# Kernel optimization log

Measured on AMD Instinct MI355X. Metric: run time of the kernel, lower is better.

The kernel has to match this reference:

```python
import jax, jax.numpy as jnp
import numpy as np


def setup_inputs() -> dict:
    key = jax.random.key(0)
    k1, k2, k3 = jax.random.split(key, 3)
    B, N, D, T = 8, 2, 256, 500
    SPK = 2000
    H = jax.random.normal(k1, (B, N, D, T), dtype=jnp.float32)
    S = jax.random.randint(k2, (B, N, T), 0, SPK, dtype=jnp.int64)
    E = jax.random.normal(k3, (SPK, D), dtype=jnp.float32)
    alpha = jnp.ones((1,), dtype=jnp.float32) * 10.0
    beta = jnp.ones((1,), dtype=jnp.float32) * 5.0
    return {"H": H, "S": S, "E": E, "alpha": alpha, "beta": beta, "N": 2}


def reference(H, S, E, alpha, beta, N):
    # H: (B, N, D, T); S: (B, N, T) int ids; E: (SPK, D)
    B, N_, D, T = H.shape
    # embedding lookup: (B, N, T, D) -> (B, N, D, T)
    E_S = jnp.transpose(E[S], (0, 1, 3, 2))
    # pairwise dist between predicted vectors and active-speaker embeddings
    # (B, N_pred=N, N_emb=N, T) -- small, direct broadcast
    Dist_p = jnp.sum((H[:, None, :, :, :] - E_S[:, :, None, :, :]) ** 2, axis=3)
    # N == 2 path matching (identity vs swap), min over the two alignments
    p0 = Dist_p[:, 0, 0, :] + Dist_p[:, 1, 1, :]  # (B, T)
    p1 = Dist_p[:, 0, 1, :] + Dist_p[:, 1, 0, :]  # (B, T)
    Dmin = jnp.minimum(p0, p1)                    # (B, T)
    Dmin = -alpha * Dmin + beta                   # broadcast (1,) over (B, T)
    # full distance to every speaker: ||H||^2 + ||E||^2 - 2 H.E
    # avoids materializing (B, SPK, N, D, T)
    Hsq = jnp.sum(H * H, axis=2)                  # (B, N, T)
    Esq = jnp.sum(E * E, axis=1)                  # (SPK,)
    cross = jnp.einsum('bndt,sd->bsnt', H, E)     # (B, SPK, N, T)
    Dist = Hsq[:, None, :, :] + Esq[None, :, None, None] - 2.0 * cross
    Dist = -alpha * Dist + beta                   # (B, SPK, N, T)
    lse = jax.nn.logsumexp(Dist, axis=1)          # (B, N, T)
    loss = -jnp.mean(Dmin) + jnp.mean(lse)
    return (E_S[:, :, :, 0], loss)
```

## Files before the change

### kernel.cpp

```cpp
#include <hip/hip_runtime.h>
#include <math.h>

#define Bb   8
#define Dd   256
#define Tt   500
#define SPK  2000
#define SPKP 2048
#define BN   16
#define L2E  1.4426950408889634f
#define LN2  0.6931471805599453f

#define EXP2F(x) __builtin_amdgcn_exp2f(x)
#define LOG2F(x) __builtin_amdgcn_logf(x)

#define F_ESN   0
#define F_HSQP  4096
#define F_PM    36864
#define F_PL    69632
#define F_DMP2  102400
#define EBF_BYTES ((size_t)167936 * 4)
#define HBF_BYTES (EBF_BYTES + (size_t)1048576)

#define ROWSTRIDE 264

typedef __bf16 v8bf __attribute__((ext_vector_type(8)));
typedef float  v4f  __attribute__((ext_vector_type(4)));

__device__ inline unsigned pack_bf16x2(float lo, float hi) {
    union { __bf16 h; unsigned short u; } a, b;
    a.h = (__bf16)lo; b.h = (__bf16)hi;
    return ((unsigned)b.u << 16) | (unsigned)a.u;
}

__global__ __launch_bounds__(256) void prep_all_kernel(
        const float* __restrict__ E, const int* __restrict__ S,
        const float* __restrict__ H, const float* __restrict__ alpha,
        const float* __restrict__ beta, float* __restrict__ ws,
        float* __restrict__ out) {
    int bid = blockIdx.x;
    int tid = threadIdx.x;

    if (bid < 512) {
        int s = bid * 4 + (tid >> 6);
        int lane = tid & 63;
        float4 v = make_float4(0.f, 0.f, 0.f, 0.f);
        if (s < SPK) v = ((const float4*)E)[s * 64 + lane];
        __bf16* ebf = (__bf16*)((char*)ws + EBF_BYTES);
        uint2 pp;
        pp.x = pack_bf16x2(v.x, v.y);
        pp.y = pack_bf16x2(v.z, v.w);
        *(uint2*)(ebf + (size_t)s * Dd + lane * 4) = pp;
        float acc = v.x * v.x + v.y * v.y + v.z * v.z + v.w * v.w;
        #pragma unroll
        for (int off = 32; off > 0; off >>= 1) acc += __shfl_down(acc, off, 64);
        if (lane == 0) ws[F_ESN + s] = (s < SPK) ? (-alpha[0] * acc * L2E) : -1e30f;
    } else if (bid < 528) {
        if (bid == 512 && tid == 0) out[BN * Dd] = 0.f;
        int i = (bid - 512) * 256 + tid;
        int bn = i >> 8, d = i & 255;
        out[i] = E[(size_t)S[bn * Tt] * Dd + d];
    } else {
        __shared__ float trans[32][65];
        int u = bid - 528;
        int bn = u >> 6;
        int r = u & 63;
        int tt0 = (r & 15) * 32;
        int d0 = (r >> 4) * 64;
        const float* Hb = H + (size_t)bn * Dd * Tt;
        #pragma unroll
        for (int p = 0; p < 8; ++p) {
            int flat = p * 256 + tid;
            int dd = flat >> 5;
            int tl = flat & 31;
            int t = tt0 + tl;
            trans[tl][dd] = (t < Tt) ? Hb[(size_t)(d0 + dd) * Tt + t] : 0.f;
        }
        __syncthreads();
        int tw = tid >> 3;
        int j = tid & 7;
        int t = tt0 + tw;
        bool ok = (t < Tt);
        int tc = ok ? t : (Tt - 1);
        int b = bn >> 1;
        int s0 = S[(b * 2 + 0) * Tt + tc];
        int s1 = S[(b * 2 + 1) * Tt + tc];
        const float4* e0p = (const float4*)(E + (size_t)s0 * Dd + d0 + j * 8);
        const float4* e1p = (const float4*)(E + (size_t)s1 * Dd + d0 + j * 8);
        float4 ea0 = e0p[0], ea1 = e0p[1];
        float4 eb0 = e1p[0], eb1 = e1p[1];
        float ev0[8] = {ea0.x, ea0.y, ea0.z, ea0.w, ea1.x, ea1.y, ea1.z, ea1.w};
        float ev1[8] = {eb0.x, eb0.y, eb0.z, eb0.w, eb1.x, eb1.y, eb1.z, eb1.w};
        float sq = 0.f, p0 = 0.f, p1 = 0.f;
        float vals[8];
        #pragma unroll
        for (int e = 0; e < 8; ++e) {
            float x = trans[tw][j * 8 + e];
            vals[e] = x;
            sq = fmaf(x, x, sq);
            float u0 = x - ev0[e]; p0 = fmaf(u0, u0, p0);
            float u1 = x - ev1[e]; p1 = fmaf(u1, u1, p1);
        }
        sq += __shfl_xor(sq, 1, 64); p0 += __shfl_xor(p0, 1, 64); p1 += __shfl_xor(p1, 1, 64);
        sq += __shfl_xor(sq, 2, 64); p0 += __shfl_xor(p0, 2, 64); p1 += __shfl_xor(p1, 2, 64);
        sq += __shfl_xor(sq, 4, 64); p0 += __shfl_xor(p0, 4, 64); p1 += __shfl_xor(p1, 4, 64);
        uint4 pk;
        pk.x = pack_bf16x2(vals[0], vals[1]);
        pk.y = pack_bf16x2(vals[2], vals[3]);
        pk.z = pack_bf16x2(vals[4], vals[5]);
        pk.w = pack_bf16x2(vals[6], vals[7]);
        __bf16* hbf = (__bf16*)((char*)ws + HBF_BYTES);
        *(uint4*)(hbf + ((size_t)(bn * 512 + t) * Dd + d0 + j * 8)) = pk;
        if (j == 0) {
            ws[F_HSQP + (size_t)(bn * 512 + t) * 4 + (r >> 4)] = sq;
            if (ok) {
                float2 pr = make_float2(p0, p1);
                *(float2*)(ws + F_DMP2 + (((size_t)bn * 512 + t) * 4 + (r >> 4)) * 2) = pr;
            }
        }
    }
}

__global__ __launch_bounds__(256, 2) void lse_mfma_kernel(
        const float* __restrict__ alpha, const float* __restrict__ beta,
        float* __restrict__ ws) {
    __shared__ __bf16 shB[64 * ROWSTRIDE];
    __shared__ __bf16 shA[4 * 16 * ROWSTRIDE];
    __shared__ float mrg_m[4][4][16], mrg_l[4][4][16];

    int bn = blockIdx.x;
    int t0 = blockIdx.y * 64;
    int mz = blockIdx.z;
    int tid = threadIdx.x;
    int lane = tid & 63;
    int n = lane & 15;
    int q = lane >> 4;
    int w = tid >> 6;

    const __bf16* ebf = (const __bf16*)((const char*)ws + EBF_BYTES);
    const __bf16* hbf = (const __bf16*)((const char*)ws + HBF_BYTES);

    #pragma unroll
    for (int p = 0; p < 8; ++p) {
        int flat = p * 256 + tid;
        int row = flat >> 5;
        int ch = flat & 31;
        uint4 vb = *(const uint4*)(hbf + ((size_t)(bn * 512 + t0 + row) * Dd + ch * 8));
        *(uint4*)(shB + row * ROWSTRIDE + ch * 8) = vb;
    }
    __syncthreads();

    v8bf bq[4][8];
    #pragma unroll
    for (int i = 0; i < 4; ++i) {
        int tloc = 16 * i + n;
        #pragma unroll
        for (int ks = 0; ks < 8; ++ks) {
            bq[i][ks] = *reinterpret_cast<const v8bf*>(&shB[tloc * ROWSTRIDE + ks * 32 + q * 8]);
        }
    }

    float A = alpha[0], Bv = beta[0];
    float ta2p = 2.f * A * L2E;
    float ctc2[4];
    #pragma unroll
    for (int i = 0; i < 4; ++i) {
        int t = t0 + 16 * i + n;
        float4 hq = *(const float4*)(ws + F_HSQP + (size_t)(bn * 512 + t) * 4);
        float hs = hq.x + hq.y + hq.z + hq.w;
        ctc2[i] = (t < Tt) ? ((Bv - A * hs) * L2E) : 0.f;
    }

    float lm[4], ll[4];
    #pragma unroll
    for (int i = 0; i < 4; ++i) { lm[i] = -INFINITY; ll[i] = 0.f; }

    __bf16* shAw = shA + w * (16 * ROWSTRIDE);

    for (int c = 0; c < 8; ++c) {
        int sbase = mz * 512 + c * 64 + w * 16;

        uint4 tmp[8];
        #pragma unroll
        for (int p = 0; p < 8; ++p) {
            int flat = p * 64 + lane;
            int row = flat >> 5;
            int ch = flat & 31;
            tmp[p] = *(const uint4*)(ebf + ((size_t)(sbase + row) * Dd + ch * 8));
        }
        #pragma unroll
        for (int p = 0; p < 8; ++p) {
            int flat = p * 64 + lane;
            int row = flat >> 5;
            int ch = flat & 31;
            *(uint4*)(shAw + row * ROWSTRIDE + ch * 8) = tmp[p];
        }
        __asm__ volatile("s_waitcnt lgkmcnt(0)" ::: "memory");

        v8bf af[8];
        #pragma unroll
        for (int ks = 0; ks < 8; ++ks) {
            af[ks] = *reinterpret_cast<const v8bf*>(&shAw[n * ROWSTRIDE + ks * 32 + q * 8]);
        }
        float4 es4 = *(const float4*)(ws + F_ESN + sbase - w * 16 + w * 16 + q * 4);

        v4f acc[4];
        #pragma unroll
        for (int i = 0; i < 4; ++i) acc[i] = (v4f){0.f, 0.f, 0.f, 0.f};
        #pragma unroll
        for (int ks = 0; ks < 8; ++ks) {
            #pragma unroll
            for (int i = 0; i < 4; ++i) {
                acc[i] = __builtin_amdgcn_mfma_f32_16x16x32_bf16(af[ks], bq[i][ks], acc[i], 0, 0, 0);
            }
        }
        float e0 = es4.x, e1 = es4.y, e2 = es4.z, e3 = es4.w;
        #pragma unroll
        for (int i = 0; i < 4; ++i) {
            float c2 = ctc2[i];
            float v0 = fmaf(ta2p, acc[i][0], c2 + e0);
            float v1 = fmaf(ta2p, acc[i][1], c2 + e1);
            float v2 = fmaf(ta2p, acc[i][2], c2 + e2);
            float v3 = fmaf(ta2p, acc[i][3], c2 + e3);
            float vm = fmaxf(fmaxf(v0, v1), fmaxf(v2, v3));
            float s = EXP2F(v0 - vm) + EXP2F(v1 - vm) + EXP2F(v2 - vm) + EXP2F(v3 - vm);
            float nm = fmaxf(lm[i], vm);
            ll[i] = ll[i] * EXP2F(lm[i] - nm) + s * EXP2F(vm - nm);
            lm[i] = nm;
        }
    }

    #pragma unroll
    for (int i = 0; i < 4; ++i) {
        float m = lm[i], l = ll[i];
        #pragma unroll
        for (int msk = 16; msk <= 32; msk <<= 1) {
            float om = __shfl_xor(m, msk, 64);
            float ol = __shfl_xor(l, msk, 64);
            float nm = fmaxf(m, om);
            l = l * EXP2F(m - nm) + ol * EXP2F(om - nm);
            m = nm;
        }
        if (q == 0) { mrg_m[w][i][n] = m; mrg_l[w][i][n] = l; }
    }
    __syncthreads();

    if (tid < 64) {
        int i = tid >> 4, cc = tid & 15;
        float m = mrg_m[0][i][cc], l = mrg_l[0][i][cc];
        #pragma unroll
        for (int wv = 1; wv < 4; ++wv) {
            float om = mrg_m[wv][i][cc], ol = mrg_l[wv][i][cc];
            float nm = fmaxf(m, om);
            l = l * EXP2F(m - nm) + ol * EXP2F(om - nm);
            m = nm;
        }
        int tw = t0 + 16 * i + cc;
        if (tw < Tt) {
            ws[F_PM + (bn * 512 + tw) * 4 + mz] = m;
            ws[F_PL + (bn * 512 + tw) * 4 + mz] = l;
        }
    }
}

__global__ __launch_bounds__(512) void final_kernel(
        const float* __restrict__ alpha, const float* __restrict__ beta,
        const float* __restrict__ ws, float* __restrict__ out) {
    __shared__ float rL[8], rD[8];
    int b = blockIdx.x;
    int tid = threadIdx.x;
    float A = alpha[0], Bv = beta[0];

    float lsum = 0.f, dsum = 0.f;
    int t = tid;
    if (t < Tt) {
        #pragma unroll
        for (int nn = 0; nn < 2; ++nn) {
            int idx = (b * 2 + nn) * 512 + t;
            float4 m4 = *(const float4*)(ws + F_PM + (size_t)idx * 4);
            float4 l4 = *(const float4*)(ws + F_PL + (size_t)idx * 4);
            float m = m4.x, l = l4.x, nm;
            nm = fmaxf(m, m4.y); l = l * EXP2F(m - nm) + l4.y * EXP2F(m4.y - nm); m = nm;
            nm = fmaxf(m, m4.z); l = l * EXP2F(m - nm) + l4.z * EXP2F(m4.z - nm); m = nm;
            nm = fmaxf(m, m4.w); l = l * EXP2F(m - nm) + l4.w * EXP2F(m4.w - nm); m = nm;
            lsum += LN2 * (m + LOG2F(l));
        }
        const float4* P0 = (const float4*)(ws + F_DMP2 + ((size_t)(2 * b + 0) * 512 + t) * 8);
        const float4* P1 = (const float4*)(ws + F_DMP2 + ((size_t)(2 * b + 1) * 512 + t) * 8);
        float4 a0 = P0[0], a1 = P0[1];
        float4 b0 = P1[0], b1 = P1[1];
        float d00 = a0.x + a0.z + a1.x + a1.z;
        float d01 = a0.y + a0.w + a1.y + a1.w;
        float d10 = b0.x + b0.z + b1.x + b1.z;
        float d11 = b0.y + b0.w + b1.y + b1.w;
        float dm = fminf(d00 + d11, d01 + d10);
        dsum = -A * dm + Bv;
    }

    int lane = tid & 63, w = tid >> 6;
    #pragma unroll
    for (int off = 32; off > 0; off >>= 1) {
        lsum += __shfl_down(lsum, off, 64);
        dsum += __shfl_down(dsum, off, 64);
    }
    if (lane == 0) { rL[w] = lsum; rD[w] = dsum; }
    __syncthreads();
    if (tid == 0) {
        float L = 0.f, D = 0.f;
        #pragma unroll
        for (int wv = 0; wv < 8; ++wv) { L += rL[wv]; D += rD[wv]; }
        atomicAdd(&out[BN * Dd], -(D / (float)(Bb * Tt)) + L / (float)(BN * Tt));
    }
}

extern "C" void kernel_launch(void* const* d_in, const int* in_sizes, int n_in,
                              void* d_out, int out_size, void* d_ws, size_t ws_size,
                              hipStream_t stream) {
    const float* H     = (const float*)d_in[0];
    const int*   S     = (const int*)d_in[1];
    const float* E     = (const float*)d_in[2];
    const float* alpha = (const float*)d_in[3];
    const float* beta  = (const float*)d_in[4];
    float* out = (float*)d_out;
    float* ws  = (float*)d_ws;

    prep_all_kernel<<<1552, 256, 0, stream>>>(E, S, H, alpha, beta, ws, out);
    lse_mfma_kernel<<<dim3(BN, 8, 4), 256, 0, stream>>>(alpha, beta, ws);
    final_kernel<<<8, 512, 0, stream>>>(alpha, beta, ws, out);
}
```

Baseline: 93.20 us.

## Double-buffer E tiles in LDS, reusing the H buffer to prefetch the next chunk

The speaker-embedding tile for the next chunk is now loaded from global memory into registers before the current chunk's MFMA and log-sum-exp work, then written to a second LDS buffer afterwards. The second buffer reuses the shB region, which is free once H has been moved into registers, and a barrier is added after that register load. This is meant to hide global-load latency behind compute instead of stalling at the start of every chunk. In exchange it needs more registers to hold the prefetched tile, which may lower occupancy.

```diff
diff --git a/kernel.cpp b/kernel.cpp
--- a/kernel.cpp
+++ b/kernel.cpp
@@ -124,7 +124,7 @@
         const float* __restrict__ alpha, const float* __restrict__ beta,
         float* __restrict__ ws) {
     __shared__ __bf16 shB[64 * ROWSTRIDE];
-    __shared__ __bf16 shA[4 * 16 * ROWSTRIDE];
+    __shared__ __bf16 shA[64 * ROWSTRIDE];
     __shared__ float mrg_m[4][4][16], mrg_l[4][4][16];
 
     int bn = blockIdx.x;
@@ -147,6 +147,25 @@
         uint4 vb = *(const uint4*)(hbf + ((size_t)(bn * 512 + t0 + row) * Dd + ch * 8));
         *(uint4*)(shB + row * ROWSTRIDE + ch * 8) = vb;
     }
+
+    __bf16* shAw = shA + w * (16 * ROWSTRIDE);
+    __bf16* shBw = shB + w * (16 * ROWSTRIDE);
+
+    {
+        int sbase = mz * 512 + w * 16;
+        uint4 t0r[8];
+        #pragma unroll
+        for (int p = 0; p < 8; ++p) {
+            int flat = p * 64 + lane, row = flat >> 5, ch = flat & 31;
+            t0r[p] = *(const uint4*)(ebf + ((size_t)(sbase + row) * Dd + ch * 8));
+        }
+        #pragma unroll
+        for (int p = 0; p < 8; ++p) {
+            int flat = p * 64 + lane, row = flat >> 5, ch = flat & 31;
+            *(uint4*)(shAw + row * ROWSTRIDE + ch * 8) = t0r[p];
+        }
+    }
+
     __syncthreads();
 
     v8bf bq[4][8];
@@ -158,6 +177,7 @@
             bq[i][ks] = *reinterpret_cast<const v8bf*>(&shB[tloc * ROWSTRIDE + ks * 32 + q * 8]);
         }
     }
+    __syncthreads();
 
     float A = alpha[0], Bv = beta[0];
     float ta2p = 2.f * A * L2E;
@@ -174,34 +194,24 @@
     #pragma unroll
     for (int i = 0; i < 4; ++i) { lm[i] = -INFINITY; ll[i] = 0.f; }
 
-    __bf16* shAw = shA + w * (16 * ROWSTRIDE);
-
-    for (int c = 0; c < 8; ++c) {
+    auto chunk = [&](const __bf16* curw, __bf16* nxtw, int c, bool last) {
         int sbase = mz * 512 + c * 64 + w * 16;
-
         uint4 tmp[8];
-        #pragma unroll
-        for (int p = 0; p < 8; ++p) {
-            int flat = p * 64 + lane;
-            int row = flat >> 5;
-            int ch = flat & 31;
-            tmp[p] = *(const uint4*)(ebf + ((size_t)(sbase + row) * Dd + ch * 8));
-        }
-        #pragma unroll
-        for (int p = 0; p < 8; ++p) {
-            int flat = p * 64 + lane;
-            int row = flat >> 5;
-            int ch = flat & 31;
-            *(uint4*)(shAw + row * ROWSTRIDE + ch * 8) = tmp[p];
-        }
-        __asm__ volatile("s_waitcnt lgkmcnt(0)" ::: "memory");
+        if (!last) {
+            int nb = sbase + 64;
+            #pragma unroll
+            for (int p = 0; p < 8; ++p) {
+                int flat = p * 64 + lane, row = flat >> 5, ch = flat & 31;
+                tmp[p] = *(const uint4*)(ebf + ((size_t)(nb + row) * Dd + ch * 8));
+            }
+        }
 
         v8bf af[8];
         #pragma unroll
         for (int ks = 0; ks < 8; ++ks) {
-            af[ks] = *reinterpret_cast<const v8bf*>(&shAw[n * ROWSTRIDE + ks * 32 + q * 8]);
-        }
-        float4 es4 = *(const float4*)(ws + F_ESN + sbase - w * 16 + w * 16 + q * 4);
+            af[ks] = *reinterpret_cast<const v8bf*>(&curw[n * ROWSTRIDE + ks * 32 + q * 8]);
+        }
+        float4 es4 = *(const float4*)(ws + F_ESN + sbase + q * 4);
 
         v4f acc[4];
         #pragma unroll
@@ -227,6 +237,19 @@
             ll[i] = ll[i] * EXP2F(lm[i] - nm) + s * EXP2F(vm - nm);
             lm[i] = nm;
         }
+
+        if (!last) {
+            #pragma unroll
+            for (int p = 0; p < 8; ++p) {
+                int flat = p * 64 + lane, row = flat >> 5, ch = flat & 31;
+                *(uint4*)(&nxtw[row * ROWSTRIDE + ch * 8]) = tmp[p];
+            }
+        }
+    };
+
+    for (int cc = 0; cc < 4; ++cc) {
+        chunk(shAw, shBw, 2 * cc, false);
+        chunk(shBw, shAw, 2 * cc + 1, cc == 3);
     }
 
     #pragma unroll
```

Measured after the change: 113.5 us. 1.22x slower.

## Pre-swizzle bf16 speaker embeddings into MFMA fragment order and load directly

Applied to the files above, without the earlier changes.

The prep kernel now writes the bf16 embedding table in the exact per-lane MFMA A-fragment order, in 16-speaker blocks by k-step. The LSE kernel then loads each A fragment with one coalesced 16-byte global load per k-step, instead of staging rows through LDS with a wait. This removes the shared-memory round trip and the LDS allocation for the A operand, which may also allow higher occupancy. The loop is unrolled by two so loads can overlap with compute, at some cost in register pressure.

```diff
diff --git a/kernel.cpp b/kernel.cpp
--- a/kernel.cpp
+++ b/kernel.cpp
@@ -45,11 +45,18 @@
         int lane = tid & 63;
         float4 v = make_float4(0.f, 0.f, 0.f, 0.f);
         if (s < SPK) v = ((const float4*)E)[s * 64 + lane];
-        __bf16* ebf = (__bf16*)((char*)ws + EBF_BYTES);
         uint2 pp;
         pp.x = pack_bf16x2(v.x, v.y);
         pp.y = pack_bf16x2(v.z, v.w);
-        *(uint2*)(ebf + (size_t)s * Dd + lane * 4) = pp;
+        {
+            int sb = s >> 4, n = s & 15;
+            int ks = lane >> 3;
+            int qq = (lane >> 1) & 3;
+            char* dst = (char*)ws + EBF_BYTES
+                      + ((((size_t)sb * 8 + ks) * 64 + qq * 16 + n) * 16)
+                      + (lane & 1) * 8;
+            *(uint2*)dst = pp;
+        }
         float acc = v.x * v.x + v.y * v.y + v.z * v.z + v.w * v.w;
         #pragma unroll
         for (int off = 32; off > 0; off >>= 1) acc += __shfl_down(acc, off, 64);
@@ -124,7 +131,6 @@
         const float* __restrict__ alpha, const float* __restrict__ beta,
         float* __restrict__ ws) {
     __shared__ __bf16 shB[64 * ROWSTRIDE];
-    __shared__ __bf16 shA[4 * 16 * ROWSTRIDE];
     __shared__ float mrg_m[4][4][16], mrg_l[4][4][16];
 
     int bn = blockIdx.x;
@@ -136,7 +142,7 @@
     int q = lane >> 4;
     int w = tid >> 6;
 
-    const __bf16* ebf = (const __bf16*)((const char*)ws + EBF_BYTES);
+    const uint4* ebf2 = (const uint4*)((const char*)ws + EBF_BYTES);
     const __bf16* hbf = (const __bf16*)((const char*)ws + HBF_BYTES);
 
     #pragma unroll
@@ -174,34 +180,18 @@
     #pragma unroll
     for (int i = 0; i < 4; ++i) { lm[i] = -INFINITY; ll[i] = 0.f; }
 
-    __bf16* shAw = shA + w * (16 * ROWSTRIDE);
-
+    #pragma unroll 2
     for (int c = 0; c < 8; ++c) {
         int sbase = mz * 512 + c * 64 + w * 16;
-
-        uint4 tmp[8];
-        #pragma unroll
-        for (int p = 0; p < 8; ++p) {
-            int flat = p * 64 + lane;
-            int row = flat >> 5;
-            int ch = flat & 31;
-            tmp[p] = *(const uint4*)(ebf + ((size_t)(sbase + row) * Dd + ch * 8));
-        }
-        #pragma unroll
-        for (int p = 0; p < 8; ++p) {
-            int flat = p * 64 + lane;
-            int row = flat >> 5;
-            int ch = flat & 31;
-            *(uint4*)(shAw + row * ROWSTRIDE + ch * 8) = tmp[p];
-        }
-        __asm__ volatile("s_waitcnt lgkmcnt(0)" ::: "memory");
-
+        int sb = mz * 32 + c * 4 + w;
+
+        const uint4* ap = ebf2 + ((size_t)sb * 8) * 64 + lane;
         v8bf af[8];
         #pragma unroll
         for (int ks = 0; ks < 8; ++ks) {
-            af[ks] = *reinterpret_cast<const v8bf*>(&shAw[n * ROWSTRIDE + ks * 32 + q * 8]);
-        }
-        float4 es4 = *(const float4*)(ws + F_ESN + sbase - w * 16 + w * 16 + q * 4);
+            af[ks] = *reinterpret_cast<const v8bf*>(ap + ks * 64);
+        }
+        float4 es4 = *(const float4*)(ws + F_ESN + sbase + q * 4);
 
         v4f acc[4];
         #pragma unroll
```

Result: no change. 93.75 us (+0.6%).
